# Kernel optimization log

Measured on AMD Instinct MI355X. Metric: run time of the kernel, lower is better.

## Reference

```python
import jax, jax.numpy as jnp
from jax import lax
import numpy as np

B, T, EPROJS, DUNITS, ATT_DIM = 32, 2048, 1024, 1024, 1024
ACONV_CHANS, ACONV_FILTS = 10, 100
SCALING = 2.0


def setup_inputs() -> dict:
    key = jax.random.key(0)
    ks = jax.random.split(key, 12)
    s = 0.02
    return {
        "enc_hs_pad": jax.random.normal(ks[0], (B, T, EPROJS), jnp.float32),
        "enc_hs_len": jax.random.randint(ks[1], (B,), T // 2, T + 1, jnp.int32),
        "dec_z": jax.random.normal(ks[2], (B, DUNITS), jnp.float32),
        "att_prev": jax.random.uniform(ks[3], (B, T), jnp.float32) / T,
        "W_enc": jax.random.normal(ks[4], (EPROJS, ATT_DIM), jnp.float32) * s,
        "b_enc": jnp.zeros((ATT_DIM,), jnp.float32),
        "W_dec": jax.random.normal(ks[5], (DUNITS, ATT_DIM), jnp.float32) * s,
        "W_att": jax.random.normal(ks[6], (ACONV_CHANS, ATT_DIM), jnp.float32) * s,
        "conv_w": jax.random.normal(ks[7], (ACONV_CHANS, 1, 2 * ACONV_FILTS + 1), jnp.float32) * s,
        "gvec_w": jax.random.normal(ks[8], (ATT_DIM,), jnp.float32) * s,
        "gvec_b": jnp.zeros((), jnp.float32),
    }


def reference(enc_hs_pad, enc_hs_len, dec_z, att_prev, W_enc, b_enc, W_dec, W_att, conv_w, gvec_w, gvec_b):
    # location conv over previous attention: (B,1,T) -> (B,C,T), 'same' padding
    pad = (conv_w.shape[-1] - 1) // 2
    att_conv = lax.conv_general_dilated(
        att_prev[:, None, :], conv_w, window_strides=(1,),
        padding=[(pad, pad)], dimension_numbers=("NCH", "OIH", "NCH"))  # (B,C,T)
    loc = jnp.einsum("bct,cd->btd", att_conv, W_att)                     # mlp_att
    enc_proj = jnp.einsum("bte,ed->btd", enc_hs_pad, W_enc) + b_enc      # pre_compute_enc_h
    dec_proj = (dec_z @ W_dec)[:, None, :]                               # (B,1,D)
    e = jnp.tanh(loc + enc_proj + dec_proj) @ gvec_w + gvec_b            # (B,T)
    mask = jnp.arange(T)[None, :] >= enc_hs_len[:, None]                 # pad mask
    e = jnp.where(mask, -jnp.inf, e)
    w = jax.nn.softmax(SCALING * e, axis=1)                              # (B,T)
    c = jnp.einsum("bt,bte->be", w, enc_hs_pad)                          # weighted sum
    return c, w
```

## Files before the change

kernel.cpp:

```cpp
#include <hip/hip_runtime.h>
#include <hip/hip_bf16.h>
#include <math.h>

#define BB 32
#define TT 2048
#define EE 1024
#define DD 1024
#define MM (BB * TT)
#define CC 10
#define FW 201

typedef __attribute__((ext_vector_type(8))) short short8;
typedef __attribute__((ext_vector_type(4))) float f32x4;
typedef __attribute__((ext_vector_type(4))) float f4;
typedef __attribute__((ext_vector_type(8))) unsigned short u16x8;
typedef unsigned short u16;

__device__ __forceinline__ u16 f2bf(float f) {
  __hip_bfloat16 h = __float2bfloat16(f);
  return *reinterpret_cast<u16*>(&h);
}
__device__ __forceinline__ float bf2f(u16 u) {
  __hip_bfloat16 h;
  *reinterpret_cast<u16*>(&h) = u;
  return __bfloat162float(h);
}
__device__ __forceinline__ float tanh_fast(float x) {
  float ex = __expf(2.f * x);
  return 1.f - 2.f * __builtin_amdgcn_rcpf(ex + 1.f);
}

__global__ void k_zero(float* __restrict__ c) {
  int i = blockIdx.x * 256 + threadIdx.x;
  c[i] = 0.f;
}

__global__ void k_cvt(const float* __restrict__ enc, u16* __restrict__ out) {
  long i = (long)blockIdx.x * 256 + threadIdx.x;
  const f4* ep = (const f4*)enc;
  f4 x = ep[2 * i], y = ep[2 * i + 1];
  u16x8 o;
  o[0] = f2bf(x[0]); o[1] = f2bf(x[1]); o[2] = f2bf(x[2]); o[3] = f2bf(x[3]);
  o[4] = f2bf(y[0]); o[5] = f2bf(y[1]); o[6] = f2bf(y[2]); o[7] = f2bf(y[3]);
  ((u16x8*)out)[i] = o;
}

__global__ void k_tw(const float* __restrict__ W, u16* __restrict__ Wt) {
  __shared__ float tile[64][65];
  int k0 = (blockIdx.x & 15) * 64;
  int n0 = (blockIdx.x >> 4) * 64;
  int tid = threadIdx.x;
  for (int i = tid; i < 4096; i += 256) {
    int r = i >> 6, cc = i & 63;
    tile[r][cc] = W[(k0 + r) * 1024 + n0 + cc];
  }
  __syncthreads();
  for (int i = tid; i < 4096; i += 256) {
    int nr = i >> 6, kc = i & 63;
    Wt[(n0 + nr) * 1024 + k0 + kc] = f2bf(tile[kc][nr]);
  }
}

__global__ void k_conv(const float* __restrict__ att_prev, const float* __restrict__ conv_w,
                       float* __restrict__ attc) {
  __shared__ float cw[CC * FW];
  __shared__ float ap[256 + 2 * 100];
  int b = blockIdx.x >> 3;
  int t0 = (blockIdx.x & 7) * 256;
  int tid = threadIdx.x;
  for (int i = tid; i < CC * FW; i += 256) cw[i] = conv_w[i];
  for (int i = tid; i < 456; i += 256) {
    int t = t0 - 100 + i;
    ap[i] = (t >= 0 && t < TT) ? att_prev[b * TT + t] : 0.f;
  }
  __syncthreads();
  float acc[CC];
#pragma unroll
  for (int c = 0; c < CC; ++c) acc[c] = 0.f;
  for (int f = 0; f < FW; ++f) {
    float x = ap[tid + f];
#pragma unroll
    for (int c = 0; c < CC; ++c) acc[c] += x * cw[c * FW + f];
  }
  int t = t0 + tid;
  float* o = attc + (size_t)(b * TT + t) * CC;
#pragma unroll
  for (int c = 0; c < CC; ++c) o[c] = acc[c];
}

__global__ __launch_bounds__(256) void k_decp(const float* __restrict__ dec_z,
                                              const float* __restrict__ W_dec,
                                              float* __restrict__ decp) {
  int b = blockIdx.x >> 4;
  int c0 = (blockIdx.x & 15) << 6;
  __shared__ float z[1024];
  __shared__ float red[4][64];
  for (int i = threadIdx.x; i < 1024; i += 256) z[i] = dec_z[(b << 10) + i];
  __syncthreads();
  int d = c0 + (threadIdx.x & 63), ks = threadIdx.x >> 6;
  float a = 0.f;
  const float* Wp = W_dec + (size_t)(ks << 8) * 1024 + d;
  const float* zp = z + (ks << 8);
#pragma unroll 4
  for (int k = 0; k < 256; ++k) a += zp[k] * Wp[(size_t)k * 1024];
  red[ks][threadIdx.x & 63] = a;
  __syncthreads();
  if (threadIdx.x < 64)
    decp[(b << 10) + c0 + threadIdx.x] =
        (red[0][threadIdx.x] + red[1][threadIdx.x]) + (red[2][threadIdx.x] + red[3][threadIdx.x]);
}

#define VM8 asm volatile("s_waitcnt vmcnt(8)" ::: "memory")
#define VM4 asm volatile("s_waitcnt vmcnt(4)" ::: "memory")
#define VM0 asm volatile("s_waitcnt vmcnt(0)" ::: "memory")

__global__ __launch_bounds__(512, 2) void k_gemm8(
    const u16* __restrict__ A, const u16* __restrict__ Bt,
    const float* __restrict__ benc, const float* __restrict__ decp,
    const float* __restrict__ attc, const float* __restrict__ watt,
    const float* __restrict__ gvec, float* __restrict__ epart) {
  extern __shared__ u16 smem[];
  u16* sA = smem;
  u16* sB = smem + 32768;

  int tid = threadIdx.x;
  int lane = tid & 63, wid = tid >> 6;
  int frl = lane & 15, fkg = lane >> 4;
  int wm = wid >> 2, wn = wid & 3;

  int orig = (blockIdx.x & 7) * 128 + (blockIdx.x >> 3);
  int bm = orig >> 2, bn = orig & 3;
  int brow = bm << 8;
  int bcol = bn << 8;
  int b = brow >> 11;

  auto stA = [&](int par, int kk, int tile) {
    u16* region = sA + ((par * 2 + kk) << 13);
    const u16* gb = A + (size_t)brow * 1024 + tile * 64 + kk * 32;
#pragma unroll
    for (int q = 0; q < 2; ++q) {
      int s = (q << 9) + tid;
      int r = s >> 2, ch = s & 3;
      int cs = ch ^ ((r >> 1) & 3);
      const u16* src = gb + (size_t)r * 1024 + (cs << 3);
      u16* dst = region + (((q << 9) + (tid & ~63)) << 3);
      __builtin_amdgcn_global_load_lds(
          (const __attribute__((address_space(1))) void*)src,
          (__attribute__((address_space(3))) void*)dst, 16, 0, 0);
    }
  };
  auto stB = [&](int par, int kk, int tile) {
    u16* region = sB + ((par * 2 + kk) << 13);
    const u16* gb = Bt + (size_t)bcol * 1024 + tile * 64 + kk * 32;
#pragma unroll
    for (int q = 0; q < 2; ++q) {
      int s = (q << 9) + tid;
      int r = s >> 2, ch = s & 3;
      int cs = ch ^ ((r >> 1) & 3);
      const u16* src = gb + (size_t)r * 1024 + (cs << 3);
      u16* dst = region + (((q << 9) + (tid & ~63)) << 3);
      __builtin_amdgcn_global_load_lds(
          (const __attribute__((address_space(1))) void*)src,
          (__attribute__((address_space(3))) void*)dst, 16, 0, 0);
    }
  };
  auto rdA = [&](int par, int kk, int mi) -> short8 {
    int row = (wm << 7) + (mi << 4) + frl;
    int g = fkg ^ ((row >> 1) & 3);
    return *(const short8*)(sA + ((par * 2 + kk) << 13) + (row << 5) + (g << 3));
  };
  auto rdB = [&](int par, int kk, int ni) -> short8 {
    int row = (wn << 6) + (ni << 4) + frl;
    int g = fkg ^ ((row >> 1) & 3);
    return *(const short8*)(sB + ((par * 2 + kk) << 13) + (row << 5) + (g << 3));
  };

  f32x4 acc[8][4];
#pragma unroll
  for (int i = 0; i < 8; ++i)
#pragma unroll
    for (int j = 0; j < 4; ++j) acc[i][j] = (f32x4){0.f, 0.f, 0.f, 0.f};
  short8 afr[4], bfr[4];

#define PH(PAR, KK, CH, STAGE, WAIT)                                          \
  {                                                                           \
    if ((CH) == 0) {                                                          \
      _Pragma("unroll") for (int ni = 0; ni < 4; ++ni)                        \
          bfr[ni] = rdB(PAR, KK, ni);                                         \
    }                                                                         \
    _Pragma("unroll") for (int i = 0; i < 4; ++i)                             \
        afr[i] = rdA(PAR, KK, (CH)*4 + i);                                    \
    STAGE;                                                                    \
    WAIT;                                                                     \
    __builtin_amdgcn_s_barrier();                                             \
    __builtin_amdgcn_s_setprio(1);                                            \
    _Pragma("unroll") for (int i = 0; i < 4; ++i)                             \
        _Pragma("unroll") for (int ni = 0; ni < 4; ++ni)                      \
            acc[(CH)*4 + i][ni] = __builtin_amdgcn_mfma_f32_16x16x32_bf16(    \
                afr[i], bfr[ni], acc[(CH)*4 + i][ni], 0, 0, 0);               \
    __builtin_amdgcn_s_setprio(0);                                            \
    __builtin_amdgcn_s_barrier();                                             \
  }

  stA(0, 0, 0); stB(0, 0, 0);
  stA(0, 1, 0); stB(0, 1, 0);
  stA(1, 0, 1); stB(1, 0, 1);
  VM8;
  __builtin_amdgcn_s_barrier();

#pragma unroll 1
  for (int I = 0; I < 7; ++I) {
    int t = 2 * I;
    PH(0, 0, 0, stA(1, 1, t + 1), ((void)0));
    PH(0, 0, 1, stB(1, 1, t + 1), VM8);
    PH(0, 1, 0, stA(0, 0, t + 2), ((void)0));
    PH(0, 1, 1, stB(0, 0, t + 2), VM8);
    PH(1, 0, 0, stA(0, 1, t + 2), ((void)0));
    PH(1, 0, 1, stB(0, 1, t + 2), VM8);
    PH(1, 1, 0, stA(1, 0, t + 3), ((void)0));
    PH(1, 1, 1, stB(1, 0, t + 3), VM8);
  }
  PH(0, 0, 0, stA(1, 1, 15), ((void)0));
  PH(0, 0, 1, stB(1, 1, 15), VM8);
  PH(0, 1, 0, ((void)0), ((void)0));
  PH(0, 1, 1, ((void)0), VM4);
  PH(1, 0, 0, ((void)0), ((void)0));
  PH(1, 0, 1, ((void)0), VM0);
  PH(1, 1, 0, ((void)0), ((void)0));
  PH(1, 1, 1, ((void)0), ((void)0));
#undef PH

  __syncthreads();
  float* fsm = (float*)smem;
  float* se_attc = fsm;
  float* se_watt = fsm + 2560;
  float* se_col  = fsm + 5120;
  float* se_g    = fsm + 5376;
  float* se_ep   = fsm + 5632;
  for (int i = tid; i < 2560; i += 512) {
    se_attc[i] = attc[(size_t)brow * 10 + i];
    se_watt[i] = watt[(i >> 8) * 1024 + bcol + (i & 255)];
  }
  if (tid < 256) {
    se_col[tid] = benc[bcol + tid] + decp[(b << 10) + bcol + tid];
    se_g[tid] = gvec[bcol + tid];
  }
  __syncthreads();

#pragma unroll
  for (int mi = 0; mi < 8; ++mi) {
#pragma unroll
    for (int j = 0; j < 4; ++j) {
      int rl = (wm << 7) + (mi << 4) + (fkg << 2) + j;
      float ar[CC];
#pragma unroll
      for (int c = 0; c < CC; ++c) ar[c] = se_attc[rl * 10 + c];
      float esum = 0.f;
#pragma unroll
      for (int ni = 0; ni < 4; ++ni) {
        int cl = (wn << 6) + (ni << 4) + frl;
        float qv = acc[mi][ni][j] + se_col[cl];
#pragma unroll
        for (int c = 0; c < CC; ++c) qv += ar[c] * se_watt[c * 256 + cl];
        esum += se_g[cl] * tanh_fast(qv);
      }
#pragma unroll
      for (int o = 8; o >= 1; o >>= 1) esum += __shfl_xor(esum, o, 16);
      if (frl == 0) se_ep[rl * 4 + wn] = esum;
    }
  }
  __syncthreads();
  if (tid < 256)
    epart[bn * MM + brow + tid] =
        (se_ep[tid * 4 + 0] + se_ep[tid * 4 + 1]) + (se_ep[tid * 4 + 2] + se_ep[tid * 4 + 3]);
}

__global__ __launch_bounds__(256) void k_softmax(const float* __restrict__ ep,
                                                 const int* __restrict__ len,
                                                 float* __restrict__ wout) {
  int b = blockIdx.x;
  int L = len[b];
  __shared__ float se[TT];
  __shared__ float red[4], red2[4];
  int tid = threadIdx.x, w = tid >> 6, lane = tid & 63;
  for (int t = tid; t < TT; t += 256) {
    int m = b * TT + t;
    se[t] = (ep[m] + ep[MM + m]) + (ep[2 * MM + m] + ep[3 * MM + m]);
  }
  __syncthreads();
  float mx = -3.4e38f;
  for (int t = tid; t < TT; t += 256)
    if (t < L) mx = fmaxf(mx, se[t]);
  for (int o = 32; o >= 1; o >>= 1) mx = fmaxf(mx, __shfl_xor(mx, o, 64));
  if (lane == 0) red[w] = mx;
  __syncthreads();
  mx = fmaxf(fmaxf(red[0], red[1]), fmaxf(red[2], red[3]));
  float s = 0.f;
  for (int t = tid; t < TT; t += 256)
    if (t < L) s += __expf(2.f * (se[t] - mx));
  for (int o = 32; o >= 1; o >>= 1) s += __shfl_xor(s, o, 64);
  if (lane == 0) red2[w] = s;
  __syncthreads();
  s = (red2[0] + red2[1]) + (red2[2] + red2[3]);
  float inv = 1.f / s;
  for (int t = tid; t < TT; t += 256)
    wout[b * TT + t] = (t < L) ? __expf(2.f * (se[t] - mx)) * inv : 0.f;
}

__global__ __launch_bounds__(256) void k_ctx(const u16* __restrict__ encbf,
                                             const float* __restrict__ wout,
                                             float* __restrict__ c) {
  int b = blockIdx.x >> 3;
  int t0 = (blockIdx.x & 7) << 8;
  int col8 = (threadIdx.x & 127) << 3;
  int rp = threadIdx.x >> 7;
  const float* wb = wout + b * TT + t0;
  float acc[8] = {0, 0, 0, 0, 0, 0, 0, 0};
  for (int tt = rp; tt < 256; tt += 2) {
    float wv = wb[tt];
    if (wv == 0.f) continue;
    u16x8 v = *(const u16x8*)(encbf + (((size_t)(b * TT + t0 + tt)) << 10) + col8);
#pragma unroll
    for (int j = 0; j < 8; ++j) acc[j] += wv * bf2f(v[j]);
  }
  __shared__ float red[128][8];
  if (rp) {
#pragma unroll
    for (int j = 0; j < 8; ++j) red[threadIdx.x & 127][j] = acc[j];
  }
  __syncthreads();
  if (!rp) {
#pragma unroll
    for (int j = 0; j < 8; ++j) acc[j] += red[threadIdx.x][j];
#pragma unroll
    for (int j = 0; j < 8; ++j) atomicAdd(&c[(b << 10) + col8 + j], acc[j]);
  }
}

extern "C" void kernel_launch(void* const* d_in, const int* in_sizes, int n_in,
                              void* d_out, int out_size, void* d_ws, size_t ws_size,
                              hipStream_t stream) {
  const float* enc = (const float*)d_in[0];
  const int* elen = (const int*)d_in[1];
  const float* dec_z = (const float*)d_in[2];
  const float* att_prev = (const float*)d_in[3];
  const float* W_enc = (const float*)d_in[4];
  const float* b_enc = (const float*)d_in[5];
  const float* W_dec = (const float*)d_in[6];
  const float* W_att = (const float*)d_in[7];
  const float* conv_w = (const float*)d_in[8];
  const float* gvec_w = (const float*)d_in[9];

  char* ws = (char*)d_ws;
  u16* encbf = (u16*)ws;    ws += (size_t)MM * EE * 2;
  u16* Wt = (u16*)ws;       ws += (size_t)EE * DD * 2;
  float* attc = (float*)ws; ws += (size_t)MM * CC * 4;
  float* decp = (float*)ws; ws += (size_t)BB * DD * 4;
  float* ep = (float*)ws;   ws += (size_t)4 * MM * 4;

  float* c = (float*)d_out;
  float* wout = c + BB * DD;

  hipFuncSetAttribute((const void*)k_gemm8,
                      hipFuncAttributeMaxDynamicSharedMemorySize, 131072);

  k_zero<<<128, 256, 0, stream>>>(c);
  k_cvt<<<(MM * EE / 8) / 256, 256, 0, stream>>>(enc, encbf);
  k_tw<<<256, 256, 0, stream>>>(W_enc, Wt);
  k_conv<<<256, 256, 0, stream>>>(att_prev, conv_w, attc);
  k_decp<<<512, 256, 0, stream>>>(dec_z, W_dec, decp);
  k_gemm8<<<1024, 512, 131072, stream>>>(encbf, Wt, b_enc, decp, attc, W_att, gvec_w, ep);
  k_softmax<<<BB, 256, 0, stream>>>(ep, elen, wout);
  k_ctx<<<256, 256, 0, stream>>>(encbf, wout, c);
}
```

Before: 715.1 us.

## Fuse prep kernels and fold location term into GEMM as extra K step

```diff
diff --git a/kernel.cpp b/kernel.cpp
--- a/kernel.cpp
+++ b/kernel.cpp
@@ -14,7 +14,9 @@
 typedef __attribute__((ext_vector_type(4))) float f32x4;
 typedef __attribute__((ext_vector_type(4))) float f4;
 typedef __attribute__((ext_vector_type(8))) unsigned short u16x8;
+typedef __attribute__((ext_vector_type(4))) unsigned int u32x4;
 typedef unsigned short u16;
+typedef unsigned int u32;
 
 __device__ __forceinline__ u16 f2bf(float f) {
   __hip_bfloat16 h = __float2bfloat16(f);
@@ -25,99 +27,123 @@
   *reinterpret_cast<u16*>(&h) = u;
   return __bfloat162float(h);
 }
+__device__ __forceinline__ u32 cvt_pk_bf16(float lo, float hi) {
+  u32 r;
+  asm("v_cvt_pk_bf16_f32 %0, %1, %2" : "=v"(r) : "v"(lo), "v"(hi));
+  return r;
+}
 __device__ __forceinline__ float tanh_fast(float x) {
   float ex = __expf(2.f * x);
   return 1.f - 2.f * __builtin_amdgcn_rcpf(ex + 1.f);
 }
 
-__global__ void k_zero(float* __restrict__ c) {
-  int i = blockIdx.x * 256 + threadIdx.x;
-  c[i] = 0.f;
-}
-
-__global__ void k_cvt(const float* __restrict__ enc, u16* __restrict__ out) {
-  long i = (long)blockIdx.x * 256 + threadIdx.x;
-  const f4* ep = (const f4*)enc;
-  f4 x = ep[2 * i], y = ep[2 * i + 1];
-  u16x8 o;
-  o[0] = f2bf(x[0]); o[1] = f2bf(x[1]); o[2] = f2bf(x[2]); o[3] = f2bf(x[3]);
-  o[4] = f2bf(y[0]); o[5] = f2bf(y[1]); o[6] = f2bf(y[2]); o[7] = f2bf(y[3]);
-  ((u16x8*)out)[i] = o;
-}
-
-__global__ void k_tw(const float* __restrict__ W, u16* __restrict__ Wt) {
+__global__ __launch_bounds__(256) void k_prep(
+    const float* __restrict__ enc, u16* __restrict__ encbf,
+    const float* __restrict__ W_enc, u16* __restrict__ Wt,
+    const float* __restrict__ att_prev, const float* __restrict__ conv_w,
+    u16* __restrict__ attc32,
+    const float* __restrict__ dec_z, const float* __restrict__ W_dec,
+    float* __restrict__ decp,
+    const float* __restrict__ W_att, u16* __restrict__ wattT,
+    float* __restrict__ c) {
+  int bid = blockIdx.x, tid = threadIdx.x;
   __shared__ float tile[64][65];
-  int k0 = (blockIdx.x & 15) * 64;
-  int n0 = (blockIdx.x >> 4) * 64;
-  int tid = threadIdx.x;
-  for (int i = tid; i < 4096; i += 256) {
-    int r = i >> 6, cc = i & 63;
-    tile[r][cc] = W[(k0 + r) * 1024 + n0 + cc];
-  }
-  __syncthreads();
-  for (int i = tid; i < 4096; i += 256) {
-    int nr = i >> 6, kc = i & 63;
-    Wt[(n0 + nr) * 1024 + k0 + kc] = f2bf(tile[kc][nr]);
-  }
-}
-
-__global__ void k_conv(const float* __restrict__ att_prev, const float* __restrict__ conv_w,
-                       float* __restrict__ attc) {
   __shared__ float cw[CC * FW];
   __shared__ float ap[256 + 2 * 100];
-  int b = blockIdx.x >> 3;
-  int t0 = (blockIdx.x & 7) * 256;
-  int tid = threadIdx.x;
-  for (int i = tid; i < CC * FW; i += 256) cw[i] = conv_w[i];
-  for (int i = tid; i < 456; i += 256) {
-    int t = t0 - 100 + i;
-    ap[i] = (t >= 0 && t < TT) ? att_prev[b * TT + t] : 0.f;
-  }
-  __syncthreads();
-  float acc[CC];
-#pragma unroll
-  for (int c = 0; c < CC; ++c) acc[c] = 0.f;
-  for (int f = 0; f < FW; ++f) {
-    float x = ap[tid + f];
-#pragma unroll
-    for (int c = 0; c < CC; ++c) acc[c] += x * cw[c * FW + f];
-  }
-  int t = t0 + tid;
-  float* o = attc + (size_t)(b * TT + t) * CC;
-#pragma unroll
-  for (int c = 0; c < CC; ++c) o[c] = acc[c];
-}
-
-__global__ __launch_bounds__(256) void k_decp(const float* __restrict__ dec_z,
-                                              const float* __restrict__ W_dec,
-                                              float* __restrict__ decp) {
-  int b = blockIdx.x >> 4;
-  int c0 = (blockIdx.x & 15) << 6;
   __shared__ float z[1024];
   __shared__ float red[4][64];
-  for (int i = threadIdx.x; i < 1024; i += 256) z[i] = dec_z[(b << 10) + i];
-  __syncthreads();
-  int d = c0 + (threadIdx.x & 63), ks = threadIdx.x >> 6;
-  float a = 0.f;
-  const float* Wp = W_dec + (size_t)(ks << 8) * 1024 + d;
-  const float* zp = z + (ks << 8);
+
+  if (bid < 4096) {
+    const f4* ep = (const f4*)enc;
+    u32x4* op = (u32x4*)encbf;
+    for (long i = (long)bid * 256 + tid; i < (long)MM * EE / 8; i += 4096 * 256) {
+      f4 x = ep[2 * i], y = ep[2 * i + 1];
+      u32x4 o;
+      o[0] = cvt_pk_bf16(x[0], x[1]);
+      o[1] = cvt_pk_bf16(x[2], x[3]);
+      o[2] = cvt_pk_bf16(y[0], y[1]);
+      o[3] = cvt_pk_bf16(y[2], y[3]);
+      op[i] = o;
+    }
+  } else if (bid < 4352) {
+    int rel = bid - 4096;
+    int k0 = (rel & 15) * 64, n0 = (rel >> 4) * 64;
+    for (int i = tid; i < 4096; i += 256) {
+      int r = i >> 6, cc = i & 63;
+      tile[r][cc] = W_enc[(k0 + r) * 1024 + n0 + cc];
+    }
+    __syncthreads();
+    for (int i = tid; i < 4096; i += 256) {
+      int nr = i >> 6, kc = i & 63;
+      Wt[(n0 + nr) * 1024 + k0 + kc] = f2bf(tile[kc][nr]);
+    }
+  } else if (bid < 4608) {
+    int rel = bid - 4352;
+    int b = rel >> 3, t0 = (rel & 7) * 256;
+    for (int i = tid; i < CC * FW; i += 256) cw[i] = conv_w[i];
+    for (int i = tid; i < 456; i += 256) {
+      int t = t0 - 100 + i;
+      ap[i] = (t >= 0 && t < TT) ? att_prev[b * TT + t] : 0.f;
+    }
+    __syncthreads();
+    float acc[CC];
+#pragma unroll
+    for (int cc = 0; cc < CC; ++cc) acc[cc] = 0.f;
+    for (int f = 0; f < FW; ++f) {
+      float x = ap[tid + f];
+#pragma unroll
+      for (int cc = 0; cc < CC; ++cc) acc[cc] += x * cw[cc * FW + f];
+    }
+    u16 row[32];
+#pragma unroll
+    for (int cc = 0; cc < CC; ++cc) row[cc] = f2bf(acc[cc]);
+#pragma unroll
+    for (int cc = CC; cc < 32; ++cc) row[cc] = 0;
+    u16x8* o = (u16x8*)(attc32 + ((size_t)(b * TT + t0 + tid) << 5));
+#pragma unroll
+    for (int q = 0; q < 4; ++q) o[q] = *(u16x8*)&row[q * 8];
+  } else if (bid < 5120) {
+    int rel = bid - 4608;
+    int b = rel >> 4, c0 = (rel & 15) << 6;
+    for (int i = tid; i < 1024; i += 256) z[i] = dec_z[(b << 10) + i];
+    __syncthreads();
+    int d = c0 + (tid & 63), ks = tid >> 6;
+    float a = 0.f;
+    const float* Wp = W_dec + (size_t)(ks << 8) * 1024 + d;
+    const float* zp = z + (ks << 8);
 #pragma unroll 4
-  for (int k = 0; k < 256; ++k) a += zp[k] * Wp[(size_t)k * 1024];
-  red[ks][threadIdx.x & 63] = a;
-  __syncthreads();
-  if (threadIdx.x < 64)
-    decp[(b << 10) + c0 + threadIdx.x] =
-        (red[0][threadIdx.x] + red[1][threadIdx.x]) + (red[2][threadIdx.x] + red[3][threadIdx.x]);
+    for (int k = 0; k < 256; ++k) a += zp[k] * Wp[(size_t)k * 1024];
+    red[ks][tid & 63] = a;
+    __syncthreads();
+    if (tid < 64)
+      decp[(b << 10) + c0 + tid] =
+          (red[0][tid] + red[1][tid]) + (red[2][tid] + red[3][tid]);
+  } else if (bid < 5248) {
+    c[(bid - 5120) * 256 + tid] = 0.f;
+  } else {
+    int n0 = (bid - 5248) << 6;
+    if (tid < 64) {
+      int n = n0 + tid;
+      u16 row[32];
+#pragma unroll
+      for (int k = 0; k < CC; ++k) row[k] = f2bf(W_att[k * 1024 + n]);
+#pragma unroll
+      for (int k = CC; k < 32; ++k) row[k] = 0;
+      u16x8* o = (u16x8*)(wattT + ((size_t)n << 5));
+#pragma unroll
+      for (int q = 0; q < 4; ++q) o[q] = *(u16x8*)&row[q * 8];
+    }
+  }
 }
 
 #define VM8 asm volatile("s_waitcnt vmcnt(8)" ::: "memory")
-#define VM4 asm volatile("s_waitcnt vmcnt(4)" ::: "memory")
+#define VM2 asm volatile("s_waitcnt vmcnt(2)" ::: "memory")
 #define VM0 asm volatile("s_waitcnt vmcnt(0)" ::: "memory")
 
 __global__ __launch_bounds__(512, 2) void k_gemm8(
     const u16* __restrict__ A, const u16* __restrict__ Bt,
+    const u16* __restrict__ attc32, const u16* __restrict__ wattT,
     const float* __restrict__ benc, const float* __restrict__ decp,
-    const float* __restrict__ attc, const float* __restrict__ watt,
     const float* __restrict__ gvec, float* __restrict__ epart) {
   extern __shared__ u16 smem[];
   u16* sA = smem;
@@ -134,35 +160,24 @@
   int bcol = bn << 8;
   int b = brow >> 11;
 
-  auto stA = [&](int par, int kk, int tile) {
-    u16* region = sA + ((par * 2 + kk) << 13);
-    const u16* gb = A + (size_t)brow * 1024 + tile * 64 + kk * 32;
+  auto stage = [&](u16* region, const u16* srcbase, int stride) {
 #pragma unroll
     for (int q = 0; q < 2; ++q) {
       int s = (q << 9) + tid;
       int r = s >> 2, ch = s & 3;
       int cs = ch ^ ((r >> 1) & 3);
-      const u16* src = gb + (size_t)r * 1024 + (cs << 3);
+      const u16* src = srcbase + (size_t)r * stride + (cs << 3);
       u16* dst = region + (((q << 9) + (tid & ~63)) << 3);
       __builtin_amdgcn_global_load_lds(
           (const __attribute__((address_space(1))) void*)src,
           (__attribute__((address_space(3))) void*)dst, 16, 0, 0);
     }
   };
+  auto stA = [&](int par, int kk, int tile) {
+    stage(sA + ((par * 2 + kk) << 13), A + (size_t)brow * 1024 + tile * 64 + kk * 32, 1024);
+  };
   auto stB = [&](int par, int kk, int tile) {
-    u16* region = sB + ((par * 2 + kk) << 13);
-    const u16* gb = Bt + (size_t)bcol * 1024 + tile * 64 + kk * 32;
-#pragma unroll
-    for (int q = 0; q < 2; ++q) {
-      int s = (q << 9) + tid;
-      int r = s >> 2, ch = s & 3;
-      int cs = ch ^ ((r >> 1) & 3);
-      const u16* src = gb + (size_t)r * 1024 + (cs << 3);
-      u16* dst = region + (((q << 9) + (tid & ~63)) << 3);
-      __builtin_amdgcn_global_load_lds(
-          (const __attribute__((address_space(1))) void*)src,
-          (__attribute__((address_space(3))) void*)dst, 16, 0, 0);
-    }
+    stage(sB + ((par * 2 + kk) << 13), Bt + (size_t)bcol * 1024 + tile * 64 + kk * 32, 1024);
   };
   auto rdA = [&](int par, int kk, int mi) -> short8 {
     int row = (wm << 7) + (mi << 4) + frl;
@@ -223,56 +238,53 @@
   PH(0, 0, 0, stA(1, 1, 15), ((void)0));
   PH(0, 0, 1, stB(1, 1, 15), VM8);
   PH(0, 1, 0, ((void)0), ((void)0));
-  PH(0, 1, 1, ((void)0), VM4);
-  PH(1, 0, 0, ((void)0), ((void)0));
-  PH(1, 0, 1, ((void)0), VM0);
+  PH(0, 1, 1, ((void)0), VM2);
+  PH(1, 0, 0, stage(sA, attc32 + ((size_t)brow << 5), 32), ((void)0));
+  PH(1, 0, 1, stage(sB, wattT + ((size_t)bcol << 5), 32), VM2);
   PH(1, 1, 0, ((void)0), ((void)0));
-  PH(1, 1, 1, ((void)0), ((void)0));
+  PH(1, 1, 1, ((void)0), VM0);
 #undef PH
 
-  __syncthreads();
-  float* fsm = (float*)smem;
-  float* se_attc = fsm;
-  float* se_watt = fsm + 2560;
-  float* se_col  = fsm + 5120;
-  float* se_g    = fsm + 5376;
-  float* se_ep   = fsm + 5632;
-  for (int i = tid; i < 2560; i += 512) {
-    se_attc[i] = attc[(size_t)brow * 10 + i];
-    se_watt[i] = watt[(i >> 8) * 1024 + bcol + (i & 255)];
-  }
-  if (tid < 256) {
-    se_col[tid] = benc[bcol + tid] + decp[(b << 10) + bcol + tid];
-    se_g[tid] = gvec[bcol + tid];
-  }
-  __syncthreads();
-
+  {
+    short8 a2[8], b2[4];
+#pragma unroll
+    for (int ni = 0; ni < 4; ++ni) b2[ni] = rdB(0, 0, ni);
+#pragma unroll
+    for (int mi = 0; mi < 8; ++mi) a2[mi] = rdA(0, 0, mi);
+#pragma unroll
+    for (int mi = 0; mi < 8; ++mi)
+#pragma unroll
+      for (int ni = 0; ni < 4; ++ni)
+        acc[mi][ni] = __builtin_amdgcn_mfma_f32_16x16x32_bf16(a2[mi], b2[ni], acc[mi][ni], 0, 0, 0);
+  }
+
+  float* se_ep = (float*)(sB + (3 << 13));
+  float colv[4], gv[4];
+#pragma unroll
+  for (int ni = 0; ni < 4; ++ni) {
+    int cl = bcol + (wn << 6) + (ni << 4) + frl;
+    colv[ni] = benc[cl] + decp[(b << 10) + cl];
+    gv[ni] = gvec[cl];
+  }
 #pragma unroll
   for (int mi = 0; mi < 8; ++mi) {
 #pragma unroll
     for (int j = 0; j < 4; ++j) {
       int rl = (wm << 7) + (mi << 4) + (fkg << 2) + j;
-      float ar[CC];
-#pragma unroll
-      for (int c = 0; c < CC; ++c) ar[c] = se_attc[rl * 10 + c];
       float esum = 0.f;
 #pragma unroll
-      for (int ni = 0; ni < 4; ++ni) {
-        int cl = (wn << 6) + (ni << 4) + frl;
-        float qv = acc[mi][ni][j] + se_col[cl];
-#pragma unroll
-        for (int c = 0; c < CC; ++c) qv += ar[c] * se_watt[c * 256 + cl];
-        esum += se_g[cl] * tanh_fast(qv);
-      }
+      for (int ni = 0; ni < 4; ++ni)
+        esum += gv[ni] * tanh_fast(acc[mi][ni][j] + colv[ni]);
 #pragma unroll
       for (int o = 8; o >= 1; o >>= 1) esum += __shfl_xor(esum, o, 16);
-      if (frl == 0) se_ep[rl * 4 + wn] = esum;
+      if (frl == 0) se_ep[(rl << 2) + wn] = esum;
     }
   }
   __syncthreads();
   if (tid < 256)
     epart[bn * MM + brow + tid] =
-        (se_ep[tid * 4 + 0] + se_ep[tid * 4 + 1]) + (se_ep[tid * 4 + 2] + se_ep[tid * 4 + 3]);
+        (se_ep[(tid << 2) + 0] + se_ep[(tid << 2) + 1]) +
+        (se_ep[(tid << 2) + 2] + se_ep[(tid << 2) + 3]);
 }
 
 __global__ __launch_bounds__(256) void k_softmax(const float* __restrict__ ep,
@@ -310,13 +322,13 @@
 __global__ __launch_bounds__(256) void k_ctx(const u16* __restrict__ encbf,
                                              const float* __restrict__ wout,
                                              float* __restrict__ c) {
-  int b = blockIdx.x >> 3;
-  int t0 = (blockIdx.x & 7) << 8;
+  int b = blockIdx.x >> 4;
+  int t0 = (blockIdx.x & 15) << 7;
   int col8 = (threadIdx.x & 127) << 3;
   int rp = threadIdx.x >> 7;
   const float* wb = wout + b * TT + t0;
   float acc[8] = {0, 0, 0, 0, 0, 0, 0, 0};
-  for (int tt = rp; tt < 256; tt += 2) {
+  for (int tt = rp; tt < 128; tt += 2) {
     float wv = wb[tt];
     if (wv == 0.f) continue;
     u16x8 v = *(const u16x8*)(encbf + (((size_t)(b * TT + t0 + tt)) << 10) + col8);
@@ -354,7 +366,8 @@
   char* ws = (char*)d_ws;
   u16* encbf = (u16*)ws;    ws += (size_t)MM * EE * 2;
   u16* Wt = (u16*)ws;       ws += (size_t)EE * DD * 2;
-  float* attc = (float*)ws; ws += (size_t)MM * CC * 4;
+  u16* attc32 = (u16*)ws;   ws += (size_t)MM * 32 * 2;
+  u16* wattT = (u16*)ws;    ws += (size_t)DD * 32 * 2;
   float* decp = (float*)ws; ws += (size_t)BB * DD * 4;
   float* ep = (float*)ws;   ws += (size_t)4 * MM * 4;
 
@@ -364,12 +377,10 @@
   hipFuncSetAttribute((const void*)k_gemm8,
                       hipFuncAttributeMaxDynamicSharedMemorySize, 131072);
 
-  k_zero<<<128, 256, 0, stream>>>(c);
-  k_cvt<<<(MM * EE / 8) / 256, 256, 0, stream>>>(enc, encbf);
-  k_tw<<<256, 256, 0, stream>>>(W_enc, Wt);
-  k_conv<<<256, 256, 0, stream>>>(att_prev, conv_w, attc);
-  k_decp<<<512, 256, 0, stream>>>(dec_z, W_dec, decp);
-  k_gemm8<<<1024, 512, 131072, stream>>>(encbf, Wt, b_enc, decp, attc, W_att, gvec_w, ep);
+  k_prep<<<5264, 256, 0, stream>>>(enc, encbf, W_enc, Wt, att_prev, conv_w,
+                                   attc32, dec_z, W_dec, decp, W_att, wattT, c);
+  k_gemm8<<<1024, 512, 131072, stream>>>(encbf, Wt, attc32, wattT, b_enc, decp,
+                                         gvec_w, ep);
   k_softmax<<<BB, 256, 0, stream>>>(ep, elen, wout);
-  k_ctx<<<256, 256, 0, stream>>>(encbf, wout, c);
-}
+  k_ctx<<<512, 256, 0, stream>>>(encbf, wout, c);
+}
```

Result: faster. 619.0 us (-13.4%).
